# Performance work log

Hardware: AMD Instinct MI355X
Metric: run time of the kernel (lower is better)

## Reference

```python
import jax, jax.numpy as jnp
import numpy as np

D_MODEL = 768
N_HEADS_CFG = 12
D_STATE = 32
D_CONV = 4
EXPAND = 2
HEADDIM = D_MODEL // N_HEADS_CFG          # 64
D_INNER = EXPAND * D_MODEL                # 1536
NHEADS = D_INNER // HEADDIM               # 24 (Mamba2 internal heads)
CONV_DIM = D_INNER + 2 * D_STATE          # 1600
D_IN_PROJ = 2 * D_INNER + 2 * D_STATE + NHEADS  # 3160
EPS = 1e-5
B_SZ, SEQ = 2, 512


def rmsnorm(x, w):
    return x * jax.lax.rsqrt(jnp.mean(x * x, axis=-1, keepdims=True) + EPS) * w


def mamba2(u, Wi, cw, cb, dtb, Alog, Dp, nw, Wo):
    """Mamba2 mixer: in_proj -> causal depthwise conv(silu) -> selective scan -> gated RMSNorm -> out_proj."""
    b, l, _ = u.shape
    zxbcdt = u @ Wi.T                                   # [b,l,d_in_proj]
    z, xBC, dt = jnp.split(zxbcdt, [D_INNER, D_INNER + CONV_DIM], axis=-1)
    # causal depthwise conv over time
    xBC = jnp.transpose(xBC, (0, 2, 1))                 # [b,c,l]
    xBC = jax.lax.conv_general_dilated(
        xBC, cw[:, None, :], window_strides=(1,),
        padding=[(D_CONV - 1, 0)], feature_group_count=CONV_DIM)
    xBC = jax.nn.silu(jnp.transpose(xBC + cb[None, :, None], (0, 2, 1)))
    x, Bm, Cm = jnp.split(xBC, [D_INNER, D_INNER + D_STATE], axis=-1)
    x = x.reshape(b, l, NHEADS, HEADDIM)                # [b,l,h,p]
    dt = jax.nn.softplus(dt + dtb)                      # [b,l,h]
    A = -jnp.exp(Alog)                                  # [h]
    a = jnp.exp(dt * A)                                 # decay [b,l,h]
    # dt * x outer B  -> [b,l,h,p,n]
    dBx = (dt[..., None, None] * x[..., None]) * Bm[:, :, None, None, :]

    def combine(e1, e2):
        a1, h1 = e1
        a2, h2 = e2
        return (a1 * a2, a2[..., None, None] * h1 + h2)

    _, h = jax.lax.associative_scan(combine, (a, dBx), axis=1)  # h: [b,l,h,p,n]
    y = jnp.einsum('blhpn,bln->blhp', h, Cm) + Dp[None, None, :, None] * x
    y = y.reshape(b, l, D_INNER)
    y = rmsnorm(y * jax.nn.silu(z), nw)                 # gated RMSNorm
    return y @ Wo.T                                     # [b,l,d_model]


def _mamba_params(key, scale=0.02):
    ks = jax.random.split(key, 6)
    return dict(
        in_w=jax.random.normal(ks[0], (D_IN_PROJ, D_MODEL), jnp.float32) * scale,
        conv_w=jax.random.normal(ks[1], (CONV_DIM, D_CONV), jnp.float32) * scale,
        conv_b=jnp.zeros((CONV_DIM,), jnp.float32),
        dt_bias=jax.random.uniform(ks[2], (NHEADS,), jnp.float32, -4.0, -1.0),
        A_log=jnp.log(jax.random.uniform(ks[3], (NHEADS,), jnp.float32, 1.0, 16.0)),
        D=jnp.ones((NHEADS,), jnp.float32),
        norm_w=jnp.ones((D_INNER,), jnp.float32),
        out_w=jax.random.normal(ks[4], (D_MODEL, D_INNER), jnp.float32) * scale,
    )


def setup_inputs() -> dict:
    key = jax.random.key(0)
    kx, kf, kb, ko = jax.random.split(key, 4)
    f = _mamba_params(kf)
    bw = _mamba_params(kb)
    return {
        'x': jax.random.normal(kx, (B_SZ, SEQ, D_MODEL), jnp.float32),
        'norm_w': jnp.ones((D_MODEL,), jnp.float32),
        'fwd_in_w': f['in_w'], 'fwd_conv_w': f['conv_w'], 'fwd_conv_b': f['conv_b'],
        'fwd_dt_bias': f['dt_bias'], 'fwd_A_log': f['A_log'], 'fwd_D': f['D'],
        'fwd_norm_w': f['norm_w'], 'fwd_out_w': f['out_w'],
        'bwd_in_w': bw['in_w'], 'bwd_conv_w': bw['conv_w'], 'bwd_conv_b': bw['conv_b'],
        'bwd_dt_bias': bw['dt_bias'], 'bwd_A_log': bw['A_log'], 'bwd_D': bw['D'],
        'bwd_norm_w': bw['norm_w'], 'bwd_out_w': bw['out_w'],
        'out_proj_w': jax.random.normal(ko, (D_MODEL, 2 * D_MODEL), jnp.float32) * 0.02,
    }


def reference(x, norm_w,
              fwd_in_w, fwd_conv_w, fwd_conv_b, fwd_dt_bias, fwd_A_log, fwd_D, fwd_norm_w, fwd_out_w,
              bwd_in_w, bwd_conv_w, bwd_conv_b, bwd_dt_bias, bwd_A_log, bwd_D, bwd_norm_w, bwd_out_w,
              out_proj_w):
    h = rmsnorm(x, norm_w)
    f_out = mamba2(h, fwd_in_w, fwd_conv_w, fwd_conv_b, fwd_dt_bias, fwd_A_log, fwd_D, fwd_norm_w, fwd_out_w)
    b_out = mamba2(h[:, ::-1], bwd_in_w, bwd_conv_w, bwd_conv_b, bwd_dt_bias, bwd_A_log, bwd_D, bwd_norm_w, bwd_out_w)[:, ::-1]
    return x + jnp.concatenate([f_out, b_out], axis=-1) @ out_proj_w.T
```

## Files before the change

### kernel.cpp

```cpp
#include <hip/hip_runtime.h>
#include <hip/hip_bf16.h>

#define DMODEL 768
#define DINNER 1536
#define DSTATE 32
#define NHEADS 24
#define HEADDIM 64
#define CONVDIM 1600
#define DINPROJ 3160
#define NPAD 3200
#define SEQ 512
#define MROWS 1024
#define CL 64
#define NCH 8

typedef __attribute__((ext_vector_type(8))) short bf16x8;
typedef __attribute__((ext_vector_type(4))) float f32x4;

__device__ __forceinline__ ushort f2bs(float v) {
  __hip_bfloat16 b = __float2bfloat16(v);
  return __builtin_bit_cast(unsigned short, b);
}
__device__ __forceinline__ float b2f(ushort u) {
  return __uint_as_float(((uint)u) << 16);
}

__device__ __forceinline__ void gld16(const void* g, const void* l) {
  __builtin_amdgcn_global_load_lds((const __attribute__((address_space(1))) void*)g,
                                   (__attribute__((address_space(3))) void*)l, 16, 0, 0);
}

__device__ __forceinline__ void wait_vm(int n) {
  switch (n) {
    case 0: asm volatile("s_waitcnt vmcnt(0)" ::: "memory"); break;
    case 2: asm volatile("s_waitcnt vmcnt(2)" ::: "memory"); break;
    case 3: asm volatile("s_waitcnt vmcnt(3)" ::: "memory"); break;
    case 4: asm volatile("s_waitcnt vmcnt(4)" ::: "memory"); break;
    default: asm volatile("s_waitcnt vmcnt(6)" ::: "memory"); break;
  }
}

__device__ __forceinline__ float block_reduce_sum(float v, float* ws4) {
#pragma unroll
  for (int o = 32; o > 0; o >>= 1) v += __shfl_xor(v, o, 64);
  int wid = threadIdx.x >> 6;
  if ((threadIdx.x & 63) == 0) ws4[wid] = v;
  __syncthreads();
  return ws4[0] + ws4[1] + ws4[2] + ws4[3];
}

__global__ __launch_bounds__(256) void prep_kernel(
    const float* __restrict__ x, const float* __restrict__ w, ushort* __restrict__ h,
    const float* __restrict__ s0, const float* __restrict__ s1,
    const float* __restrict__ s2, const float* __restrict__ s3,
    const float* __restrict__ s4, ushort* __restrict__ d) {
  if (blockIdx.x < MROWS) {
    __shared__ float ws4[4];
    int m = blockIdx.x;
    const float* xr = x + (size_t)m * DMODEL;
    float v[3];
    float ss = 0.f;
#pragma unroll
    for (int i = 0; i < 3; ++i) {
      v[i] = xr[threadIdx.x + i * 256];
      ss += v[i] * v[i];
    }
    ss = block_reduce_sum(ss, ws4);
    float sc = rsqrtf(ss / (float)DMODEL + 1e-5f);
    ushort* hr = h + (size_t)m * DMODEL;
#pragma unroll
    for (int i = 0; i < 3; ++i) {
      int c = threadIdx.x + i * 256;
      hr[c] = f2bs(v[i] * sc * w[c]);
    }
    return;
  }
  constexpr size_t NP_IN = (size_t)NPAD * DMODEL;
  constexpr size_t NE_IN = (size_t)DINPROJ * DMODEL;
  constexpr size_t NE_O = (size_t)DMODEL * DINNER;
  size_t i = (((size_t)blockIdx.x - MROWS) * 256 + threadIdx.x) * 4;
  const float* src;
  size_t off, ne;
  if (i < NP_IN) { src = s0; off = i; ne = NE_IN; }
  else if (i < 2 * NP_IN) { src = s1; off = i - NP_IN; ne = NE_IN; }
  else if (i < 2 * NP_IN + NE_O) { src = s2; off = i - 2 * NP_IN; ne = NE_O; }
  else if (i < 2 * NP_IN + 2 * NE_O) { src = s3; off = i - 2 * NP_IN - NE_O; ne = NE_O; }
  else if (i < 2 * NP_IN + 3 * NE_O) { src = s4; off = i - 2 * NP_IN - 2 * NE_O; ne = NE_O; }
  else return;
  ushort* dp = d + i;
  if (off + 3 < ne) {
    float4 v = *(const float4*)(src + off);
    dp[0] = f2bs(v.x); dp[1] = f2bs(v.y); dp[2] = f2bs(v.z); dp[3] = f2bs(v.w);
  } else {
#pragma unroll
    for (int j = 0; j < 4; ++j) dp[j] = (off + j < ne) ? f2bs(src[off + j]) : (ushort)0;
  }
}

template <int BM, int BN, bool ADD_X, bool OUT_BF16>
__global__ __launch_bounds__(256) void gemm5(
    const ushort* __restrict__ A, int lda, size_t aZ,
    const ushort* __restrict__ Bw, int ldb, size_t bZ,
    void* __restrict__ Cout, int ldc, size_t cZ,
    const float* __restrict__ X, int ldx, int K) {
  constexpr int AG = BM / 16;
  constexpr int BG = BN / 16;
  constexpr int LPT = (AG + BG) / 4;
  constexpr int MR = BM / 32;
  constexpr int NR = BN / 32;
  __shared__ ushort As[3][BM * 32];
  __shared__ ushort Bs[3][BN * 32];
  const int t = threadIdx.x, w = t >> 6, l = t & 63;
  int bx, by;
  {
    int gx = gridDim.x, gy = gridDim.y;
    int nwg = gx * gy;
    int flat = blockIdx.y * gx + blockIdx.x;
    int s = (flat & 7) * (nwg >> 3) + (flat >> 3);
    bx = s / gy; by = s % gy;
  }
  const int m0 = by * BM, n0 = bx * BN;
  const int wr = w >> 1, wc = w & 1;
  const int fr = l & 15, fq = l >> 4;
  const int sr = l >> 2, sc2 = (l & 3) * 8;
  const ushort* Ap = A + (size_t)blockIdx.z * aZ;
  const ushort* Bp = Bw + (size_t)blockIdx.z * bZ;

  auto stage = [&](int bb, int k0) {
#pragma unroll
    for (int g = w; g < AG + BG; g += 4) {
      if (g < AG)
        gld16(Ap + (size_t)(m0 + g * 16 + sr) * lda + k0 + sc2, (const char*)&As[bb][0] + g * 1024);
      else
        gld16(Bp + (size_t)(n0 + (g - AG) * 16 + sr) * ldb + k0 + sc2,
              (const char*)&Bs[bb][0] + (g - AG) * 1024);
    }
  };

  f32x4 acc[MR][NR];
#pragma unroll
  for (int m = 0; m < MR; ++m)
#pragma unroll
    for (int n = 0; n < NR; ++n) acc[m][n] = (f32x4){0.f, 0.f, 0.f, 0.f};

  const int nk = K / 32;
  stage(0, 0);
  stage(1, 32);
  stage(2, 64);
  int b = 0;
  for (int k = 0; k < nk; ++k) {
    int rem = nk - 1 - k;
    wait_vm(LPT * (rem < 2 ? rem : 2));
    __builtin_amdgcn_sched_barrier(0);
    __builtin_amdgcn_s_barrier();
    __builtin_amdgcn_sched_barrier(0);
    bf16x8 af[MR], bfr[NR];
#pragma unroll
    for (int m = 0; m < MR; ++m)
      af[m] = *(const bf16x8*)&As[b][(wr * (BM / 2) + m * 16 + fr) * 32 + fq * 8];
#pragma unroll
    for (int n = 0; n < NR; ++n)
      bfr[n] = *(const bf16x8*)&Bs[b][(wc * (BN / 2) + n * 16 + fr) * 32 + fq * 8];
#pragma unroll
    for (int m = 0; m < MR; ++m)
#pragma unroll
      for (int n = 0; n < NR; ++n)
        acc[m][n] = __builtin_amdgcn_mfma_f32_16x16x32_bf16(af[m], bfr[n], acc[m][n], 0, 0, 0);
    __builtin_amdgcn_sched_barrier(0);
    __builtin_amdgcn_s_barrier();
    if (k + 3 < nk) stage(b, (k + 3) * 32);
    b = (b == 2) ? 0 : b + 1;
  }

#pragma unroll
  for (int m = 0; m < MR; ++m) {
#pragma unroll
    for (int n = 0; n < NR; ++n) {
      int col = n0 + wc * (BN / 2) + n * 16 + fr;
#pragma unroll
      for (int j = 0; j < 4; ++j) {
        int row = m0 + wr * (BM / 2) + m * 16 + fq * 4 + j;
        float v = acc[m][n][j];
        if (ADD_X) v += X[(size_t)row * ldx + col];
        if (OUT_BF16)
          ((ushort*)Cout + (size_t)blockIdx.z * cZ)[(size_t)row * ldc + col] = f2bs(v);
        else
          ((float*)Cout + (size_t)blockIdx.z * cZ)[(size_t)row * ldc + col] = v;
      }
    }
  }
}

__global__ __launch_bounds__(256) void conv_dt_kernel(
    const ushort* __restrict__ zxb,
    const float* __restrict__ cw0, const float* __restrict__ cb0,
    const float* __restrict__ dtb0, const float* __restrict__ Al0,
    const float* __restrict__ cw1, const float* __restrict__ cb1,
    const float* __restrict__ dtb1, const float* __restrict__ Al1,
    ushort* __restrict__ xbc, float* __restrict__ dta) {
  int m = blockIdx.x;
  int dir = blockIdx.y;
  int l = m & (SEQ - 1);
  const float* cw = dir ? cw1 : cw0;
  const float* cb = dir ? cb1 : cb0;
  const ushort* zrow = zxb + (size_t)m * 6400 + dir * 3200 + DINNER;
  ushort* xo = xbc + ((size_t)dir * MROWS + m) * CONVDIM;
  for (int c = threadIdx.x; c < CONVDIM; c += 256) {
    float acc = cb[c];
    if (dir == 0) {
#pragma unroll
      for (int d = 0; d < 4; ++d) {
        if (l - d >= 0) acc = fmaf(b2f(zrow[-(ptrdiff_t)d * 6400 + c]), cw[c * 4 + 3 - d], acc);
      }
    } else {
#pragma unroll
      for (int d = 0; d < 4; ++d) {
        if (l + d < SEQ) acc = fmaf(b2f(zrow[(ptrdiff_t)d * 6400 + c]), cw[c * 4 + 3 - d], acc);
      }
    }
    xo[c] = f2bs(acc / (1.f + expf(-acc)));
  }
  if (threadIdx.x < NHEADS) {
    int hh = threadIdx.x;
    const float* dtb = dir ? dtb1 : dtb0;
    const float* Al = dir ? Al1 : Al0;
    float v = b2f(zxb[(size_t)m * 6400 + dir * 3200 + DINNER + CONVDIM + hh]) + dtb[hh];
    float dt = (v > 20.f) ? v : log1pf(expf(v));
    float A = -expf(Al[hh]);
    dta[((size_t)dir * MROWS + m) * 48 + hh] = dt;
    dta[((size_t)dir * MROWS + m) * 48 + NHEADS + hh] = expf(dt * A);
  }
}

__device__ __forceinline__ void scan_stage(
    const ushort* __restrict__ xb, int c, int dir, int h, int t,
    float xs[CL][64], float bcs[CL][64]) {
#pragma unroll
  for (int i = 0; i < 4; ++i) {
    int slot = t + i * 256;
    int s = slot >> 4, seg = (slot >> 3) & 1, o8 = slot & 7;
    int tau = c * CL + s;
    int prow = dir ? (SEQ - 1 - tau) : tau;
    const ushort* rp = xb + (size_t)prow * CONVDIM + (seg ? DINNER : h * HEADDIM) + o8 * 8;
    uint4 u = *(const uint4*)rp;
    float* dst = seg ? &bcs[s][o8 * 8] : &xs[s][o8 * 8];
    uint ua[4] = {u.x, u.y, u.z, u.w};
#pragma unroll
    for (int j = 0; j < 4; ++j) {
      dst[j * 2] = __uint_as_float((ua[j] & 0xffffu) << 16);
      dst[j * 2 + 1] = __uint_as_float(ua[j] & 0xffff0000u);
    }
  }
}

__global__ __launch_bounds__(256) void scan_phase1(
    const ushort* __restrict__ xbc, const float* __restrict__ dta,
    float* __restrict__ sbuf, float* __restrict__ abuf) {
  __shared__ float xs[CL][64];
  __shared__ float bcs[CL][64];
  __shared__ float das[CL][2];
  int c = blockIdx.x, bh = blockIdx.y, dir = blockIdx.z;
  int b = bh / NHEADS, h = bh % NHEADS;
  int t = threadIdx.x, p = t >> 2, q = t & 3;
  const ushort* xb = xbc + ((size_t)dir * MROWS + b * SEQ) * CONVDIM;
  scan_stage(xb, c, dir, h, t, xs, bcs);
  if (t < 128) {
    int s = t >> 1, wsel = t & 1;
    int tau = c * CL + s;
    int prow = dir ? (SEQ - 1 - tau) : tau;
    das[s][wsel] = dta[((size_t)dir * MROWS + b * SEQ + prow) * 48 + wsel * NHEADS + h];
  }
  __syncthreads();
  float hst[8];
#pragma unroll
  for (int j = 0; j < 8; ++j) hst[j] = 0.f;
  float alpha = 1.f;
#pragma unroll 8
  for (int s = 0; s < CL; ++s) {
    float xp = xs[s][p];
    float dt_s = das[s][0], a_s = das[s][1];
    float cx = dt_s * xp;
    alpha *= a_s;
    float4 B0 = *(const float4*)&bcs[s][q * 8];
    float4 B1 = *(const float4*)&bcs[s][q * 8 + 4];
    float Bv[8] = {B0.x, B0.y, B0.z, B0.w, B1.x, B1.y, B1.z, B1.w};
#pragma unroll
    for (int j = 0; j < 8; ++j) hst[j] = fmaf(a_s, hst[j], cx * Bv[j]);
  }
  float* sp = sbuf + (((size_t)(dir * 48 + bh)) * NCH + c) * 2048 + p * 32 + q * 8;
  *(float4*)sp = (float4){hst[0], hst[1], hst[2], hst[3]};
  *(float4*)(sp + 4) = (float4){hst[4], hst[5], hst[6], hst[7]};
  if (t == 0) abuf[(dir * 48 + bh) * NCH + c] = alpha;
}

__global__ __launch_bounds__(256) void scan_phase3b(
    const ushort* __restrict__ xbc, const float* __restrict__ dta,
    const float* __restrict__ sbuf, const float* __restrict__ abuf,
    const float* __restrict__ Dp0, const float* __restrict__ Dp1,
    float* __restrict__ y) {
  __shared__ float xs[CL][64];
  __shared__ float bcs[CL][64];
  __shared__ float das[CL][2];
  int c = blockIdx.x, bh = blockIdx.y, dir = blockIdx.z;
  int b = bh / NHEADS, h = bh % NHEADS;
  int t = threadIdx.x, p = t >> 2, q = t & 3;
  const ushort* xb = xbc + ((size_t)dir * MROWS + b * SEQ) * CONVDIM;
  scan_stage(xb, c, dir, h, t, xs, bcs);
  if (t < 128) {
    int s = t >> 1, wsel = t & 1;
    int tau = c * CL + s;
    int prow = dir ? (SEQ - 1 - tau) : tau;
    das[s][wsel] = dta[((size_t)dir * MROWS + b * SEQ + prow) * 48 + wsel * NHEADS + h];
  }

  float hst[8];
#pragma unroll
  for (int j = 0; j < 8; ++j) hst[j] = 0.f;
  for (int cc = 0; cc < c; ++cc) {
    const float* sp = sbuf + (((size_t)(dir * 48 + bh)) * NCH + cc) * 2048 + p * 32 + q * 8;
    float4 s0 = *(const float4*)sp;
    float4 s1 = *(const float4*)(sp + 4);
    float al = abuf[(dir * 48 + bh) * NCH + cc];
    float sv[8] = {s0.x, s0.y, s0.z, s0.w, s1.x, s1.y, s1.z, s1.w};
#pragma unroll
    for (int j = 0; j < 8; ++j) hst[j] = fmaf(al, hst[j], sv[j]);
  }

  float Dv = (dir ? Dp1 : Dp0)[h];
  __syncthreads();
#pragma unroll 8
  for (int s = 0; s < CL; ++s) {
    float xp = xs[s][p];
    float dt_s = das[s][0], a_s = das[s][1];
    float cx = dt_s * xp;
    float4 B0 = *(const float4*)&bcs[s][q * 8];
    float4 B1 = *(const float4*)&bcs[s][q * 8 + 4];
    float4 C0 = *(const float4*)&bcs[s][32 + q * 8];
    float4 C1 = *(const float4*)&bcs[s][32 + q * 8 + 4];
    float Bv[8] = {B0.x, B0.y, B0.z, B0.w, B1.x, B1.y, B1.z, B1.w};
    float Cv[8] = {C0.x, C0.y, C0.z, C0.w, C1.x, C1.y, C1.z, C1.w};
    float acc = 0.f;
#pragma unroll
    for (int j = 0; j < 8; ++j) {
      hst[j] = fmaf(a_s, hst[j], cx * Bv[j]);
      acc = fmaf(hst[j], Cv[j], acc);
    }
    acc += __shfl_xor(acc, 1, 64);
    acc += __shfl_xor(acc, 2, 64);
    if (q == 0) {
      int tau = c * CL + s;
      int prow = dir ? (SEQ - 1 - tau) : tau;
      y[((size_t)dir * MROWS + b * SEQ + prow) * DINNER + h * HEADDIM + p] = fmaf(Dv, xp, acc);
    }
  }
}

__global__ __launch_bounds__(256) void gated_norm_kernel(
    const float* __restrict__ y,
    const ushort* __restrict__ zxb,
    const float* __restrict__ nw0, const float* __restrict__ nw1,
    ushort* __restrict__ yn) {
  __shared__ float ws4[4];
  int m = blockIdx.x;
  int dir = blockIdx.y;
  const float* nw = dir ? nw1 : nw0;
  float g[6];
  float ss = 0.f;
#pragma unroll
  for (int i = 0; i < 6; ++i) {
    int c = threadIdx.x + i * 256;
    float yv = y[((size_t)dir * MROWS + m) * DINNER + c];
    float zv = b2f(zxb[(size_t)m * 6400 + dir * 3200 + c]);
    float gg = yv * (zv / (1.f + expf(-zv)));
    g[i] = gg;
    ss += gg * gg;
  }
  ss = block_reduce_sum(ss, ws4);
  float sc = rsqrtf(ss / (float)DINNER + 1e-5f);
#pragma unroll
  for (int i = 0; i < 6; ++i) {
    int c = threadIdx.x + i * 256;
    yn[((size_t)dir * MROWS + m) * DINNER + c] = f2bs(g[i] * sc * nw[c]);
  }
}

extern "C" void kernel_launch(void* const* d_in, const int* in_sizes, int n_in,
                              void* d_out, int out_size, void* d_ws, size_t ws_size,
                              hipStream_t stream) {
  const float* x = (const float*)d_in[0];
  const float* norm_w = (const float*)d_in[1];
  const float* in_w[2] = {(const float*)d_in[2], (const float*)d_in[10]};
  const float* conv_w[2] = {(const float*)d_in[3], (const float*)d_in[11]};
  const float* conv_b[2] = {(const float*)d_in[4], (const float*)d_in[12]};
  const float* dt_bias[2] = {(const float*)d_in[5], (const float*)d_in[13]};
  const float* A_log[2] = {(const float*)d_in[6], (const float*)d_in[14]};
  const float* Dp[2] = {(const float*)d_in[7], (const float*)d_in[15]};
  const float* nw[2] = {(const float*)d_in[8], (const float*)d_in[16]};
  const float* out_w[2] = {(const float*)d_in[9], (const float*)d_in[17]};
  const float* proj_w = (const float*)d_in[18];
  float* out = (float*)d_out;

  char* p = (char*)d_ws;
  ushort* zxb = (ushort*)p; p += (size_t)MROWS * 6400 * 2;
  ushort* xbc = (ushort*)p; p += (size_t)2 * MROWS * CONVDIM * 2;
  float* dta = (float*)p;   p += (size_t)2 * MROWS * 48 * 4;
  float* y = (float*)p;     p += (size_t)2 * MROWS * DINNER * 4;
  float* sbuf = (float*)p;  p += (size_t)96 * NCH * 2048 * 4;
  float* abuf = (float*)p;  p += (size_t)96 * NCH * 4;
  ushort* h = (ushort*)p;   p += (size_t)MROWS * DMODEL * 2;
  ushort* yn = (ushort*)p;  p += (size_t)2 * MROWS * DINNER * 2;
  ushort* cat = (ushort*)p; p += (size_t)MROWS * DINNER * 2;
  ushort* wi = (ushort*)p;  p += (size_t)2 * NPAD * DMODEL * 2;
  ushort* wo = (ushort*)p;  p += (size_t)2 * DMODEL * DINNER * 2;
  ushort* wp = (ushort*)p;  p += (size_t)DMODEL * DINNER * 2;

  {
    size_t tot = 2 * (size_t)NPAD * DMODEL + 3 * (size_t)DMODEL * DINNER;
    int fblocks = (int)((tot / 4 + 255) / 256);
    prep_kernel<<<MROWS + fblocks, 256, 0, stream>>>(x, norm_w, h, in_w[0], in_w[1],
                                                     out_w[0], out_w[1], proj_w, wi);
  }

  {
    dim3 g(6400 / 128, MROWS / 64, 1);
    gemm5<64, 128, false, true><<<g, 256, 0, stream>>>(h, DMODEL, 0, wi, DMODEL, 0,
                                                       zxb, 6400, 0, nullptr, 0, DMODEL);
  }

  conv_dt_kernel<<<dim3(MROWS, 2), 256, 0, stream>>>(
      zxb, conv_w[0], conv_b[0], dt_bias[0], A_log[0],
      conv_w[1], conv_b[1], dt_bias[1], A_log[1], xbc, dta);

  scan_phase1<<<dim3(NCH, 48, 2), 256, 0, stream>>>(xbc, dta, sbuf, abuf);
  scan_phase3b<<<dim3(NCH, 48, 2), 256, 0, stream>>>(xbc, dta, sbuf, abuf, Dp[0], Dp[1], y);

  gated_norm_kernel<<<dim3(MROWS, 2), 256, 0, stream>>>(y, zxb, nw[0], nw[1], yn);

  {
    dim3 g(DMODEL / 64, MROWS / 64, 2);
    gemm5<64, 64, false, true><<<g, 256, 0, stream>>>(
        yn, DINNER, (size_t)MROWS * DINNER, wo, DINNER, (size_t)DMODEL * DINNER,
        cat, DINNER, (size_t)DMODEL, nullptr, 0, DINNER);
  }

  {
    dim3 g(DMODEL / 64, MROWS / 64, 1);
    gemm5<64, 64, true, false><<<g, 256, 0, stream>>>(cat, DINNER, 0, wp, DINNER, 0,
                                                      out, DMODEL, 0, x, DMODEL, DINNER);
  }
}
```

Baseline: 125.2 us.

## Fuse causal conv and dt softplus into scan kernels, enlarge in_proj GEMM tile

Removes the separate conv_dt kernel and its xbc/dta intermediates. Each scan block now loads raw zxb rows for its chunk, plus a 3-row halo, into LDS and computes the depthwise conv, SiLU, softplus dt and decay in place. The in_proj GEMM moves to a 128x128 tile, and wait_vm gains a vmcnt(8) case, presumably for the deeper pipeline of the larger tile. This drops a launch and a global round trip. In exchange the conv is computed twice (phase1 and phase3), LDS use per block grows, and the GEMM grid shrinks.

Result: slower. 153.8 us (+22.8%).

```diff
diff --git a/kernel.cpp b/kernel.cpp
--- a/kernel.cpp
+++ b/kernel.cpp
@@ -36,7 +36,8 @@
     case 2: asm volatile("s_waitcnt vmcnt(2)" ::: "memory"); break;
     case 3: asm volatile("s_waitcnt vmcnt(3)" ::: "memory"); break;
     case 4: asm volatile("s_waitcnt vmcnt(4)" ::: "memory"); break;
-    default: asm volatile("s_waitcnt vmcnt(6)" ::: "memory"); break;
+    case 6: asm volatile("s_waitcnt vmcnt(6)" ::: "memory"); break;
+    default: asm volatile("s_waitcnt vmcnt(8)" ::: "memory"); break;
   }
 }
 
@@ -191,98 +192,87 @@
   }
 }
 
-__global__ __launch_bounds__(256) void conv_dt_kernel(
+struct ScanLds {
+  ushort raw[68][128];
+  float xs[CL][64];
+  float bcs[CL][64];
+  float das[CL][2];
+};
+
+__device__ __forceinline__ void scan_stage_conv(
+    ScanLds& S, const ushort* __restrict__ zxb,
+    const float* __restrict__ cw, const float* __restrict__ cb,
+    const float* __restrict__ dtb, const float* __restrict__ Al,
+    int c, int b, int h, int dir, int t) {
+  int r0 = dir ? (SEQ - 1 - c * CL - (CL - 1)) : (c * CL - 3);
+  const ushort* zb = zxb + (size_t)(b * SEQ) * 6400 + dir * 3200 + DINNER;
+#pragma unroll
+  for (int i = 0; i < 5; ++i) {
+    int slot = i * 256 + t;
+    if (slot < 67 * 16) {
+      int j = slot >> 4, seg = (slot >> 3) & 1, o = slot & 7;
+      int gr = r0 + j;
+      uint4 val = (uint4){0u, 0u, 0u, 0u};
+      if (gr >= 0 && gr < SEQ)
+        val = *(const uint4*)(zb + (size_t)gr * 6400 + (seg ? DINNER : h * HEADDIM) + o * 8);
+      *(uint4*)&S.raw[j][seg * 64 + o * 8] = val;
+    }
+  }
+  if (t < CL) {
+    int tau = c * CL + t;
+    int prow = dir ? (SEQ - 1 - tau) : tau;
+    float v = b2f(zxb[(size_t)(b * SEQ + prow) * 6400 + dir * 3200 + DINNER + CONVDIM + h]) + dtb[h];
+    float dt = (v > 20.f) ? v : log1pf(expf(v));
+    float A = -expf(Al[h]);
+    S.das[t][0] = dt;
+    S.das[t][1] = expf(dt * A);
+  }
+  __syncthreads();
+#pragma unroll 4
+  for (int i = 0; i < 32; ++i) {
+    int idx = i * 256 + t;
+    int s = idx >> 7, ch = idx & 127;
+    int cc = (ch < 64) ? (h * HEADDIM + ch) : (DINNER + ch - 64);
+    float acc = cb[cc];
+#pragma unroll
+    for (int d = 0; d < 4; ++d) {
+      if (c * CL + s - d >= 0) {
+        int rj = dir ? (63 - s + d) : (s + 3 - d);
+        acc = fmaf(b2f(S.raw[rj][ch]), cw[cc * 4 + 3 - d], acc);
+      }
+    }
+    float sv = acc / (1.f + expf(-acc));
+    if (ch < 64) S.xs[s][ch] = sv;
+    else S.bcs[s][ch - 64] = sv;
+  }
+  __syncthreads();
+}
+
+__global__ __launch_bounds__(256) void scan_p1(
     const ushort* __restrict__ zxb,
     const float* __restrict__ cw0, const float* __restrict__ cb0,
     const float* __restrict__ dtb0, const float* __restrict__ Al0,
     const float* __restrict__ cw1, const float* __restrict__ cb1,
     const float* __restrict__ dtb1, const float* __restrict__ Al1,
-    ushort* __restrict__ xbc, float* __restrict__ dta) {
-  int m = blockIdx.x;
-  int dir = blockIdx.y;
-  int l = m & (SEQ - 1);
-  const float* cw = dir ? cw1 : cw0;
-  const float* cb = dir ? cb1 : cb0;
-  const ushort* zrow = zxb + (size_t)m * 6400 + dir * 3200 + DINNER;
-  ushort* xo = xbc + ((size_t)dir * MROWS + m) * CONVDIM;
-  for (int c = threadIdx.x; c < CONVDIM; c += 256) {
-    float acc = cb[c];
-    if (dir == 0) {
-#pragma unroll
-      for (int d = 0; d < 4; ++d) {
-        if (l - d >= 0) acc = fmaf(b2f(zrow[-(ptrdiff_t)d * 6400 + c]), cw[c * 4 + 3 - d], acc);
-      }
-    } else {
-#pragma unroll
-      for (int d = 0; d < 4; ++d) {
-        if (l + d < SEQ) acc = fmaf(b2f(zrow[(ptrdiff_t)d * 6400 + c]), cw[c * 4 + 3 - d], acc);
-      }
-    }
-    xo[c] = f2bs(acc / (1.f + expf(-acc)));
-  }
-  if (threadIdx.x < NHEADS) {
-    int hh = threadIdx.x;
-    const float* dtb = dir ? dtb1 : dtb0;
-    const float* Al = dir ? Al1 : Al0;
-    float v = b2f(zxb[(size_t)m * 6400 + dir * 3200 + DINNER + CONVDIM + hh]) + dtb[hh];
-    float dt = (v > 20.f) ? v : log1pf(expf(v));
-    float A = -expf(Al[hh]);
-    dta[((size_t)dir * MROWS + m) * 48 + hh] = dt;
-    dta[((size_t)dir * MROWS + m) * 48 + NHEADS + hh] = expf(dt * A);
-  }
-}
-
-__device__ __forceinline__ void scan_stage(
-    const ushort* __restrict__ xb, int c, int dir, int h, int t,
-    float xs[CL][64], float bcs[CL][64]) {
-#pragma unroll
-  for (int i = 0; i < 4; ++i) {
-    int slot = t + i * 256;
-    int s = slot >> 4, seg = (slot >> 3) & 1, o8 = slot & 7;
-    int tau = c * CL + s;
-    int prow = dir ? (SEQ - 1 - tau) : tau;
-    const ushort* rp = xb + (size_t)prow * CONVDIM + (seg ? DINNER : h * HEADDIM) + o8 * 8;
-    uint4 u = *(const uint4*)rp;
-    float* dst = seg ? &bcs[s][o8 * 8] : &xs[s][o8 * 8];
-    uint ua[4] = {u.x, u.y, u.z, u.w};
-#pragma unroll
-    for (int j = 0; j < 4; ++j) {
-      dst[j * 2] = __uint_as_float((ua[j] & 0xffffu) << 16);
-      dst[j * 2 + 1] = __uint_as_float(ua[j] & 0xffff0000u);
-    }
-  }
-}
-
-__global__ __launch_bounds__(256) void scan_phase1(
-    const ushort* __restrict__ xbc, const float* __restrict__ dta,
     float* __restrict__ sbuf, float* __restrict__ abuf) {
-  __shared__ float xs[CL][64];
-  __shared__ float bcs[CL][64];
-  __shared__ float das[CL][2];
+  __shared__ ScanLds S;
   int c = blockIdx.x, bh = blockIdx.y, dir = blockIdx.z;
   int b = bh / NHEADS, h = bh % NHEADS;
   int t = threadIdx.x, p = t >> 2, q = t & 3;
-  const ushort* xb = xbc + ((size_t)dir * MROWS + b * SEQ) * CONVDIM;
-  scan_stage(xb, c, dir, h, t, xs, bcs);
-  if (t < 128) {
-    int s = t >> 1, wsel = t & 1;
-    int tau = c * CL + s;
-    int prow = dir ? (SEQ - 1 - tau) : tau;
-    das[s][wsel] = dta[((size_t)dir * MROWS + b * SEQ + prow) * 48 + wsel * NHEADS + h];
-  }
-  __syncthreads();
+  scan_stage_conv(S, zxb, dir ? cw1 : cw0, dir ? cb1 : cb0, dir ? dtb1 : dtb0,
+                  dir ? Al1 : Al0, c, b, h, dir, t);
   float hst[8];
 #pragma unroll
   for (int j = 0; j < 8; ++j) hst[j] = 0.f;
   float alpha = 1.f;
 #pragma unroll 8
   for (int s = 0; s < CL; ++s) {
-    float xp = xs[s][p];
-    float dt_s = das[s][0], a_s = das[s][1];
+    float xp = S.xs[s][p];
+    float dt_s = S.das[s][0], a_s = S.das[s][1];
     float cx = dt_s * xp;
     alpha *= a_s;
-    float4 B0 = *(const float4*)&bcs[s][q * 8];
-    float4 B1 = *(const float4*)&bcs[s][q * 8 + 4];
+    float4 B0 = *(const float4*)&S.bcs[s][q * 8];
+    float4 B1 = *(const float4*)&S.bcs[s][q * 8 + 4];
     float Bv[8] = {B0.x, B0.y, B0.z, B0.w, B1.x, B1.y, B1.z, B1.w};
 #pragma unroll
     for (int j = 0; j < 8; ++j) hst[j] = fmaf(a_s, hst[j], cx * Bv[j]);
@@ -293,26 +283,21 @@
   if (t == 0) abuf[(dir * 48 + bh) * NCH + c] = alpha;
 }
 
-__global__ __launch_bounds__(256) void scan_phase3b(
-    const ushort* __restrict__ xbc, const float* __restrict__ dta,
+__global__ __launch_bounds__(256) void scan_p3(
+    const ushort* __restrict__ zxb,
+    const float* __restrict__ cw0, const float* __restrict__ cb0,
+    const float* __restrict__ dtb0, const float* __restrict__ Al0,
+    const float* __restrict__ cw1, const float* __restrict__ cb1,
+    const float* __restrict__ dtb1, const float* __restrict__ Al1,
     const float* __restrict__ sbuf, const float* __restrict__ abuf,
     const float* __restrict__ Dp0, const float* __restrict__ Dp1,
     float* __restrict__ y) {
-  __shared__ float xs[CL][64];
-  __shared__ float bcs[CL][64];
-  __shared__ float das[CL][2];
+  __shared__ ScanLds S;
   int c = blockIdx.x, bh = blockIdx.y, dir = blockIdx.z;
   int b = bh / NHEADS, h = bh % NHEADS;
   int t = threadIdx.x, p = t >> 2, q = t & 3;
-  const ushort* xb = xbc + ((size_t)dir * MROWS + b * SEQ) * CONVDIM;
-  scan_stage(xb, c, dir, h, t, xs, bcs);
-  if (t < 128) {
-    int s = t >> 1, wsel = t & 1;
-    int tau = c * CL + s;
-    int prow = dir ? (SEQ - 1 - tau) : tau;
-    das[s][wsel] = dta[((size_t)dir * MROWS + b * SEQ + prow) * 48 + wsel * NHEADS + h];
-  }
-
+  scan_stage_conv(S, zxb, dir ? cw1 : cw0, dir ? cb1 : cb0, dir ? dtb1 : dtb0,
+                  dir ? Al1 : Al0, c, b, h, dir, t);
   float hst[8];
 #pragma unroll
   for (int j = 0; j < 8; ++j) hst[j] = 0.f;
@@ -325,18 +310,16 @@
 #pragma unroll
     for (int j = 0; j < 8; ++j) hst[j] = fmaf(al, hst[j], sv[j]);
   }
-
   float Dv = (dir ? Dp1 : Dp0)[h];
-  __syncthreads();
 #pragma unroll 8
   for (int s = 0; s < CL; ++s) {
-    float xp = xs[s][p];
-    float dt_s = das[s][0], a_s = das[s][1];
+    float xp = S.xs[s][p];
+    float dt_s = S.das[s][0], a_s = S.das[s][1];
     float cx = dt_s * xp;
-    float4 B0 = *(const float4*)&bcs[s][q * 8];
-    float4 B1 = *(const float4*)&bcs[s][q * 8 + 4];
-    float4 C0 = *(const float4*)&bcs[s][32 + q * 8];
-    float4 C1 = *(const float4*)&bcs[s][32 + q * 8 + 4];
+    float4 B0 = *(const float4*)&S.bcs[s][q * 8];
+    float4 B1 = *(const float4*)&S.bcs[s][q * 8 + 4];
+    float4 C0 = *(const float4*)&S.bcs[s][32 + q * 8];
+    float4 C1 = *(const float4*)&S.bcs[s][32 + q * 8 + 4];
     float Bv[8] = {B0.x, B0.y, B0.z, B0.w, B1.x, B1.y, B1.z, B1.w};
     float Cv[8] = {C0.x, C0.y, C0.z, C0.w, C1.x, C1.y, C1.z, C1.w};
     float acc = 0.f;
@@ -402,8 +385,6 @@
 
   char* p = (char*)d_ws;
   ushort* zxb = (ushort*)p; p += (size_t)MROWS * 6400 * 2;
-  ushort* xbc = (ushort*)p; p += (size_t)2 * MROWS * CONVDIM * 2;
-  float* dta = (float*)p;   p += (size_t)2 * MROWS * 48 * 4;
   float* y = (float*)p;     p += (size_t)2 * MROWS * DINNER * 4;
   float* sbuf = (float*)p;  p += (size_t)96 * NCH * 2048 * 4;
   float* abuf = (float*)p;  p += (size_t)96 * NCH * 4;
@@ -422,17 +403,17 @@
   }
 
   {
-    dim3 g(6400 / 128, MROWS / 64, 1);
-    gemm5<64, 128, false, true><<<g, 256, 0, stream>>>(h, DMODEL, 0, wi, DMODEL, 0,
-                                                       zxb, 6400, 0, nullptr, 0, DMODEL);
-  }
-
-  conv_dt_kernel<<<dim3(MROWS, 2), 256, 0, stream>>>(
+    dim3 g(6400 / 128, MROWS / 128, 1);
+    gemm5<128, 128, false, true><<<g, 256, 0, stream>>>(h, DMODEL, 0, wi, DMODEL, 0,
+                                                        zxb, 6400, 0, nullptr, 0, DMODEL);
+  }
+
+  scan_p1<<<dim3(NCH, 48, 2), 256, 0, stream>>>(
       zxb, conv_w[0], conv_b[0], dt_bias[0], A_log[0],
-      conv_w[1], conv_b[1], dt_bias[1], A_log[1], xbc, dta);
-
-  scan_phase1<<<dim3(NCH, 48, 2), 256, 0, stream>>>(xbc, dta, sbuf, abuf);
-  scan_phase3b<<<dim3(NCH, 48, 2), 256, 0, stream>>>(xbc, dta, sbuf, abuf, Dp[0], Dp[1], y);
+      conv_w[1], conv_b[1], dt_bias[1], A_log[1], sbuf, abuf);
+  scan_p3<<<dim3(NCH, 48, 2), 256, 0, stream>>>(
+      zxb, conv_w[0], conv_b[0], dt_bias[0], A_log[0],
+      conv_w[1], conv_b[1], dt_bias[1], A_log[1], sbuf, abuf, Dp[0], Dp[1], y);
 
   gated_norm_kernel<<<dim3(MROWS, 2), 256, 0, stream>>>(y, zxb, nw[0], nw[1], yn);
 
```

## Fuse gated RMSNorm into scan epilogue and out-proj GEMM row scaling

Applied to the files above, without the earlier changes.

Removes the separate gated-norm kernel. The scan kernel now applies the SiLU(z) gate, writes bf16 gated output, and accumulates per-row sum of squares with atomics. The RMS scale is applied per row in the out-projection GEMM epilogue, and the norm weight is folded into the out-projection weights during the bf16 conversion. This cuts a launch and an fp32 intermediate round trip, at the cost of atomics and slightly different rounding.

Result: slower. 148.2 us (+18.3%).

```diff
diff --git a/kernel.cpp b/kernel.cpp
--- a/kernel.cpp
+++ b/kernel.cpp
@@ -24,6 +24,8 @@
 __device__ __forceinline__ float b2f(ushort u) {
   return __uint_as_float(((uint)u) << 16);
 }
+__device__ __forceinline__ float b2f_lo(uint u) { return __uint_as_float(u << 16); }
+__device__ __forceinline__ float b2f_hi(uint u) { return __uint_as_float(u & 0xffff0000u); }
 
 __device__ __forceinline__ void gld16(const void* g, const void* l) {
   __builtin_amdgcn_global_load_lds((const __attribute__((address_space(1))) void*)g,
@@ -36,7 +38,8 @@
     case 2: asm volatile("s_waitcnt vmcnt(2)" ::: "memory"); break;
     case 3: asm volatile("s_waitcnt vmcnt(3)" ::: "memory"); break;
     case 4: asm volatile("s_waitcnt vmcnt(4)" ::: "memory"); break;
-    default: asm volatile("s_waitcnt vmcnt(6)" ::: "memory"); break;
+    case 6: asm volatile("s_waitcnt vmcnt(6)" ::: "memory"); break;
+    default: asm volatile("s_waitcnt vmcnt(8)" ::: "memory"); break;
   }
 }
 
@@ -53,7 +56,9 @@
     const float* __restrict__ x, const float* __restrict__ w, ushort* __restrict__ h,
     const float* __restrict__ s0, const float* __restrict__ s1,
     const float* __restrict__ s2, const float* __restrict__ s3,
-    const float* __restrict__ s4, ushort* __restrict__ d) {
+    const float* __restrict__ s4,
+    const float* __restrict__ nw0, const float* __restrict__ nw1,
+    ushort* __restrict__ d, float* __restrict__ sumsq) {
   if (blockIdx.x < MROWS) {
     __shared__ float ws4[4];
     int m = blockIdx.x;
@@ -75,21 +80,30 @@
     }
     return;
   }
+  if (blockIdx.x == MROWS) {
+#pragma unroll
+    for (int i = 0; i < 8; ++i) sumsq[threadIdx.x + i * 256] = 0.f;
+  }
   constexpr size_t NP_IN = (size_t)NPAD * DMODEL;
   constexpr size_t NE_IN = (size_t)DINPROJ * DMODEL;
   constexpr size_t NE_O = (size_t)DMODEL * DINNER;
   size_t i = (((size_t)blockIdx.x - MROWS) * 256 + threadIdx.x) * 4;
   const float* src;
+  const float* fold = nullptr;
   size_t off, ne;
   if (i < NP_IN) { src = s0; off = i; ne = NE_IN; }
   else if (i < 2 * NP_IN) { src = s1; off = i - NP_IN; ne = NE_IN; }
-  else if (i < 2 * NP_IN + NE_O) { src = s2; off = i - 2 * NP_IN; ne = NE_O; }
-  else if (i < 2 * NP_IN + 2 * NE_O) { src = s3; off = i - 2 * NP_IN - NE_O; ne = NE_O; }
+  else if (i < 2 * NP_IN + NE_O) { src = s2; off = i - 2 * NP_IN; ne = NE_O; fold = nw0; }
+  else if (i < 2 * NP_IN + 2 * NE_O) { src = s3; off = i - 2 * NP_IN - NE_O; ne = NE_O; fold = nw1; }
   else if (i < 2 * NP_IN + 3 * NE_O) { src = s4; off = i - 2 * NP_IN - 2 * NE_O; ne = NE_O; }
   else return;
   ushort* dp = d + i;
   if (off + 3 < ne) {
     float4 v = *(const float4*)(src + off);
+    if (fold) {
+      v.x *= fold[(off + 0) % DINNER]; v.y *= fold[(off + 1) % DINNER];
+      v.z *= fold[(off + 2) % DINNER]; v.w *= fold[(off + 3) % DINNER];
+    }
     dp[0] = f2bs(v.x); dp[1] = f2bs(v.y); dp[2] = f2bs(v.z); dp[3] = f2bs(v.w);
   } else {
 #pragma unroll
@@ -97,12 +111,13 @@
   }
 }
 
-template <int BM, int BN, bool ADD_X, bool OUT_BF16>
+template <int BM, int BN, bool ADD_X, bool OUT_BF16, bool SCALE>
 __global__ __launch_bounds__(256) void gemm5(
     const ushort* __restrict__ A, int lda, size_t aZ,
     const ushort* __restrict__ Bw, int ldb, size_t bZ,
     void* __restrict__ Cout, int ldc, size_t cZ,
-    const float* __restrict__ X, int ldx, int K) {
+    const float* __restrict__ X, int ldx, int K,
+    const float* __restrict__ rowss) {
   constexpr int AG = BM / 16;
   constexpr int BG = BN / 16;
   constexpr int LPT = (AG + BG) / 4;
@@ -175,12 +190,16 @@
 #pragma unroll
   for (int m = 0; m < MR; ++m) {
 #pragma unroll
-    for (int n = 0; n < NR; ++n) {
-      int col = n0 + wc * (BN / 2) + n * 16 + fr;
-#pragma unroll
-      for (int j = 0; j < 4; ++j) {
-        int row = m0 + wr * (BM / 2) + m * 16 + fq * 4 + j;
+    for (int j = 0; j < 4; ++j) {
+      int row = m0 + wr * (BM / 2) + m * 16 + fq * 4 + j;
+      float sc = 1.f;
+      if (SCALE)
+        sc = rsqrtf(rowss[(size_t)blockIdx.z * MROWS + row] * (1.f / (float)DINNER) + 1e-5f);
+#pragma unroll
+      for (int n = 0; n < NR; ++n) {
+        int col = n0 + wc * (BN / 2) + n * 16 + fr;
         float v = acc[m][n][j];
+        if (SCALE) v *= sc;
         if (ADD_X) v += X[(size_t)row * ldx + col];
         if (OUT_BF16)
           ((ushort*)Cout + (size_t)blockIdx.z * cZ)[(size_t)row * ldc + col] = f2bs(v);
@@ -247,8 +266,8 @@
     uint ua[4] = {u.x, u.y, u.z, u.w};
 #pragma unroll
     for (int j = 0; j < 4; ++j) {
-      dst[j * 2] = __uint_as_float((ua[j] & 0xffffu) << 16);
-      dst[j * 2 + 1] = __uint_as_float(ua[j] & 0xffff0000u);
+      dst[j * 2] = b2f_lo(ua[j]);
+      dst[j * 2 + 1] = b2f_hi(ua[j]);
     }
   }
 }
@@ -295,15 +314,17 @@
 
 __global__ __launch_bounds__(256) void scan_phase3b(
     const ushort* __restrict__ xbc, const float* __restrict__ dta,
+    const ushort* __restrict__ zxb,
     const float* __restrict__ sbuf, const float* __restrict__ abuf,
     const float* __restrict__ Dp0, const float* __restrict__ Dp1,
-    float* __restrict__ y) {
+    ushort* __restrict__ yb, float* __restrict__ sumsq) {
   __shared__ float xs[CL][64];
   __shared__ float bcs[CL][64];
   __shared__ float das[CL][2];
+  __shared__ float wsum[4][CL];
   int c = blockIdx.x, bh = blockIdx.y, dir = blockIdx.z;
   int b = bh / NHEADS, h = bh % NHEADS;
-  int t = threadIdx.x, p = t >> 2, q = t & 3;
+  int t = threadIdx.x, p = t >> 2, q = t & 3, wv = t >> 6;
   const ushort* xb = xbc + ((size_t)dir * MROWS + b * SEQ) * CONVDIM;
   scan_stage(xb, c, dir, h, t, xs, bcs);
   if (t < 128) {
@@ -347,40 +368,28 @@
     }
     acc += __shfl_xor(acc, 1, 64);
     acc += __shfl_xor(acc, 2, 64);
+    int tau = c * CL + s;
+    int prow = dir ? (SEQ - 1 - tau) : tau;
+    float val = 0.f;
     if (q == 0) {
-      int tau = c * CL + s;
-      int prow = dir ? (SEQ - 1 - tau) : tau;
-      y[((size_t)dir * MROWS + b * SEQ + prow) * DINNER + h * HEADDIM + p] = fmaf(Dv, xp, acc);
-    }
-  }
-}
-
-__global__ __launch_bounds__(256) void gated_norm_kernel(
-    const float* __restrict__ y,
-    const ushort* __restrict__ zxb,
-    const float* __restrict__ nw0, const float* __restrict__ nw1,
-    ushort* __restrict__ yn) {
-  __shared__ float ws4[4];
-  int m = blockIdx.x;
-  int dir = blockIdx.y;
-  const float* nw = dir ? nw1 : nw0;
-  float g[6];
-  float ss = 0.f;
-#pragma unroll
-  for (int i = 0; i < 6; ++i) {
-    int c = threadIdx.x + i * 256;
-    float yv = y[((size_t)dir * MROWS + m) * DINNER + c];
-    float zv = b2f(zxb[(size_t)m * 6400 + dir * 3200 + c]);
-    float gg = yv * (zv / (1.f + expf(-zv)));
-    g[i] = gg;
-    ss += gg * gg;
-  }
-  ss = block_reduce_sum(ss, ws4);
-  float sc = rsqrtf(ss / (float)DINNER + 1e-5f);
-#pragma unroll
-  for (int i = 0; i < 6; ++i) {
-    int c = threadIdx.x + i * 256;
-    yn[((size_t)dir * MROWS + m) * DINNER + c] = f2bs(g[i] * sc * nw[c]);
+      float yv = fmaf(Dv, xp, acc);
+      float zv = b2f(zxb[(size_t)(b * SEQ + prow) * 6400 + dir * 3200 + h * HEADDIM + p]);
+      float gg = yv * (zv / (1.f + expf(-zv)));
+      yb[((size_t)dir * MROWS + b * SEQ + prow) * DINNER + h * HEADDIM + p] = f2bs(gg);
+      val = gg * gg;
+    }
+    val += __shfl_xor(val, 4, 64);
+    val += __shfl_xor(val, 8, 64);
+    val += __shfl_xor(val, 16, 64);
+    val += __shfl_xor(val, 32, 64);
+    if ((t & 63) == 0) wsum[wv][s] = val;
+  }
+  __syncthreads();
+  if (t < CL) {
+    int tau = c * CL + t;
+    int prow = dir ? (SEQ - 1 - tau) : tau;
+    float tot = wsum[0][t] + wsum[1][t] + wsum[2][t] + wsum[3][t];
+    atomicAdd(&sumsq[(size_t)dir * MROWS + b * SEQ + prow], tot);
   }
 }
 
@@ -404,11 +413,11 @@
   ushort* zxb = (ushort*)p; p += (size_t)MROWS * 6400 * 2;
   ushort* xbc = (ushort*)p; p += (size_t)2 * MROWS * CONVDIM * 2;
   float* dta = (float*)p;   p += (size_t)2 * MROWS * 48 * 4;
-  float* y = (float*)p;     p += (size_t)2 * MROWS * DINNER * 4;
+  ushort* yb = (ushort*)p;  p += (size_t)2 * MROWS * DINNER * 2;
   float* sbuf = (float*)p;  p += (size_t)96 * NCH * 2048 * 4;
   float* abuf = (float*)p;  p += (size_t)96 * NCH * 4;
+  float* sumsq = (float*)p; p += (size_t)2 * MROWS * 4;
   ushort* h = (ushort*)p;   p += (size_t)MROWS * DMODEL * 2;
-  ushort* yn = (ushort*)p;  p += (size_t)2 * MROWS * DINNER * 2;
   ushort* cat = (ushort*)p; p += (size_t)MROWS * DINNER * 2;
   ushort* wi = (ushort*)p;  p += (size_t)2 * NPAD * DMODEL * 2;
   ushort* wo = (ushort*)p;  p += (size_t)2 * DMODEL * DINNER * 2;
@@ -418,13 +427,14 @@
     size_t tot = 2 * (size_t)NPAD * DMODEL + 3 * (size_t)DMODEL * DINNER;
     int fblocks = (int)((tot / 4 + 255) / 256);
     prep_kernel<<<MROWS + fblocks, 256, 0, stream>>>(x, norm_w, h, in_w[0], in_w[1],
-                                                     out_w[0], out_w[1], proj_w, wi);
+                                                     out_w[0], out_w[1], proj_w,
+                                                     nw[0], nw[1], wi, sumsq);
   }
 
   {
     dim3 g(6400 / 128, MROWS / 64, 1);
-    gemm5<64, 128, false, true><<<g, 256, 0, stream>>>(h, DMODEL, 0, wi, DMODEL, 0,
-                                                       zxb, 6400, 0, nullptr, 0, DMODEL);
+    gemm5<64, 128, false, true, false><<<g, 256, 0, stream>>>(
+        h, DMODEL, 0, wi, DMODEL, 0, zxb, 6400, 0, nullptr, 0, DMODEL, nullptr);
   }
 
   conv_dt_kernel<<<dim3(MROWS, 2), 256, 0, stream>>>(
@@ -432,20 +442,19 @@
       conv_w[1], conv_b[1], dt_bias[1], A_log[1], xbc, dta);
 
   scan_phase1<<<dim3(NCH, 48, 2), 256, 0, stream>>>(xbc, dta, sbuf, abuf);
-  scan_phase3b<<<dim3(NCH, 48, 2), 256, 0, stream>>>(xbc, dta, sbuf, abuf, Dp[0], Dp[1], y);
-
-  gated_norm_kernel<<<dim3(MROWS, 2), 256, 0, stream>>>(y, zxb, nw[0], nw[1], yn);
+  scan_phase3b<<<dim3(NCH, 48, 2), 256, 0, stream>>>(xbc, dta, zxb, sbuf, abuf,
+                                                     Dp[0], Dp[1], yb, sumsq);
 
   {
     dim3 g(DMODEL / 64, MROWS / 64, 2);
-    gemm5<64, 64, false, true><<<g, 256, 0, stream>>>(
-        yn, DINNER, (size_t)MROWS * DINNER, wo, DINNER, (size_t)DMODEL * DINNER,
-        cat, DINNER, (size_t)DMODEL, nullptr, 0, DINNER);
+    gemm5<64, 64, false, true, true><<<g, 256, 0, stream>>>(
+        yb, DINNER, (size_t)MROWS * DINNER, wo, DINNER, (size_t)DMODEL * DINNER,
+        cat, DINNER, (size_t)DMODEL, nullptr, 0, DINNER, sumsq);
   }
 
   {
     dim3 g(DMODEL / 64, MROWS / 64, 1);
-    gemm5<64, 64, true, false><<<g, 256, 0, stream>>>(cat, DINNER, 0, wp, DINNER, 0,
-                                                      out, DMODEL, 0, x, DMODEL, DINNER);
-  }
-}
+    gemm5<64, 64, true, false, false><<<g, 256, 0, stream>>>(
+        cat, DINNER, 0, wp, DINNER, 0, out, DMODEL, 0, x, DMODEL, DINNER, nullptr);
+  }
+}
```
